# Kernel optimization log

Hardware: AMD Instinct MI355X
Metric: run time of the kernel (lower is better)

The kernel has to match this reference:

```python
import jax, jax.numpy as jnp
import numpy as np

N = 100000          # num nodes
E_C = 6_400_000     # connection edges
E_D = 400_000       # destination edges
F_IN = 5
H = 8
BN_EPS = 1e-5
L2_EPS = 1e-12


def setup_inputs() -> dict:
    key = jax.random.key(0)
    ks = jax.random.split(key, 16)
    d = {}
    d["x"] = jax.random.normal(ks[0], (N, F_IN), dtype=jnp.float32)
    d["edge_index_connections"] = jax.random.randint(ks[1], (2, E_C), 0, N, dtype=jnp.int64)
    d["edge_index_destinations"] = jax.random.randint(ks[2], (2, E_D), 0, N, dtype=jnp.int64)
    # SAGEConv weights: lin_l (neighbor aggregate), lin_r (root), no bias
    d["W1l"] = jax.random.normal(ks[3], (H, F_IN), jnp.float32) * 0.3
    d["W1r"] = jax.random.normal(ks[4], (H, F_IN), jnp.float32) * 0.3
    d["W2l"] = jax.random.normal(ks[5], (H, H), jnp.float32) * 0.3
    d["W2r"] = jax.random.normal(ks[6], (H, H), jnp.float32) * 0.3
    d["W3l"] = jax.random.normal(ks[7], (H, H), jnp.float32) * 0.3
    d["W3r"] = jax.random.normal(ks[8], (H, H), jnp.float32) * 0.3
    d["W4l"] = jax.random.normal(ks[9], (H, H), jnp.float32) * 0.3
    d["W4r"] = jax.random.normal(ks[10], (H, H), jnp.float32) * 0.3
    # LazyBatchNorm1d affine params (init gamma=1, beta=0)
    for i in range(1, 5):
        d[f"g{i}"] = jnp.ones((H,), jnp.float32)
        d[f"b{i}"] = jnp.zeros((H,), jnp.float32)
    return d


def _sage(x, ei, Wl, Wr):
    # PyG SAGEConv(mean aggr, normalize=True, bias=False):
    # out = lin_l(mean_{j in N(i)} x_j) + lin_r(x_i); then L2 normalize rows.
    src, dst = ei[0], ei[1]
    msgs = x[src]                                            # [E, F] gather
    s = jax.ops.segment_sum(msgs, dst, num_segments=N)       # [N, F]
    cnt = jax.ops.segment_sum(jnp.ones((ei.shape[1],), x.dtype), dst, num_segments=N)
    mean = s / jnp.maximum(cnt, 1.0)[:, None]                # zero for isolated nodes
    out = mean @ Wl.T + x @ Wr.T                             # [N, H]
    nrm = jnp.linalg.norm(out, axis=-1, keepdims=True)
    return out / jnp.maximum(nrm, L2_EPS)


def _bn(x, g, b):
    # BatchNorm1d in training mode: per-feature batch stats (biased variance)
    m = x.mean(axis=0)
    v = x.var(axis=0)
    return (x - m) * jax.lax.rsqrt(v + BN_EPS) * g + b


def reference(x, edge_index_connections, edge_index_destinations,
              W1l, W1r, W2l, W2r, W3l, W3r, W4l, W4r,
              g1, b1, g2, b2, g3, b3, g4, b4):
    eic = edge_index_connections
    eid = edge_index_destinations
    h = _bn(jax.nn.relu(_sage(x, eic, W1l, W1r)), g1, b1)
    # ITERATIONS_BEFORE_DESTINATION = 1 (conv4 + bn2)
    h = _bn(jax.nn.relu(_sage(h, eic, W4l, W4r)), g2, b2)
    # destination pass (conv2 + bn3)
    h = _bn(jax.nn.relu(_sage(h, eid, W2l, W2r)), g3, b3)
    # ITERATIONS_AFTER_DESTINATION = 2 (conv3 + bn4)
    for _ in range(2):
        h = _bn(jax.nn.relu(_sage(h, eic, W3l, W3r)), g4, b4)
    return h
```

## Files before the change

### kernel.cpp

```cpp
#include <hip/hip_runtime.h>
#include <hip/hip_fp16.h>

#define NN 100000
#define EC 6400000
#define ED 400000
#define BN_EPS 1e-5f
#define NSB ((NN + 255) >> 8)
#define NCH 256
#define CSR_CAP 19200
#define CHUNK_OF(E) (((((E) + NCH - 1) / NCH) + 3) & ~3)


__global__ __launch_bounds__(1024)
void pre_hist_prep(const int* __restrict__ eic, const int* __restrict__ eid,
                   int* __restrict__ bhist_c, int* __restrict__ bhist_d,
                   const float* __restrict__ x, const float* __restrict__ W1l,
                   const float* __restrict__ W1r, float* __restrict__ xp,
                   __half* __restrict__ xp16,
                   float* __restrict__ W1lp, float* __restrict__ W1rp) {
    int blk = blockIdx.x;
    if (blk < 2 * NCH) {
        const int* ei = (blk < NCH) ? eic : eid;
        int E = (blk < NCH) ? EC : ED;
        int* bhist = (blk < NCH) ? bhist_c : bhist_d;
        int k = (blk < NCH) ? blk : blk - NCH;
        __shared__ int h[NSB];
        for (int i = threadIdx.x; i < NSB; i += 1024) h[i] = 0;
        __syncthreads();
        int chunk = CHUNK_OF(E);
        int beg = k * chunk, end = min(E, beg + chunk);
        for (int e = beg + threadIdx.x * 4; e < end; e += 1024 * 4) {
            int4 d4 = *(const int4*)&ei[E + e];
            atomicAdd(&h[d4.x >> 8], 1);
            atomicAdd(&h[d4.y >> 8], 1);
            atomicAdd(&h[d4.z >> 8], 1);
            atomicAdd(&h[d4.w >> 8], 1);
        }
        __syncthreads();
        for (int i = threadIdx.x; i < NSB; i += 1024) bhist[i * NCH + k] = h[i];
    } else {
        int pb = blk - 2 * NCH;
        int t = pb * 1024 + threadIdx.x;
        if (t < 64) {
            int f = t >> 3, k = t & 7;
            W1lp[t] = (k < 5) ? W1l[f * 5 + k] : 0.f;
            W1rp[t] = (k < 5) ? W1r[f * 5 + k] : 0.f;
        }
        for (int idx = t; idx < NN * 8; idx += 32 * 1024) {
            int f = idx & 7, i = idx >> 3;
            float v = (f < 5) ? x[i * 5 + f] : 0.f;
            xp[idx] = v;
            xp16[idx] = __float2half(v);
        }
    }
}

__global__ __launch_bounds__(256)
void row_scan2(int* __restrict__ bhist_c, int* __restrict__ total_c,
               int* __restrict__ bhist_d, int* __restrict__ total_d) {
    int blk = blockIdx.x;
    int* row = (blk < NSB) ? (bhist_c + blk * NCH)
                           : (bhist_d + (blk - NSB) * NCH);
    int* total = (blk < NSB) ? total_c : total_d;
    int bb = (blk < NSB) ? blk : blk - NSB;
    __shared__ int wsum[4];
    int lane = threadIdx.x & 63, w = threadIdx.x >> 6;
    int v = row[threadIdx.x];
    int x = v;
    #pragma unroll
    for (int sh = 1; sh < 64; sh <<= 1) { int y = __shfl_up(x, sh); if (lane >= sh) x += y; }
    if (lane == 63) wsum[w] = x;
    __syncthreads();
    int wb = 0;
    #pragma unroll
    for (int j = 0; j < 4; ++j) if (j < w) wb += wsum[j];
    row[threadIdx.x] = wb + x - v;
    if (threadIdx.x == 255) total[bb] = wb + x;
}

__global__ void base2(const int* __restrict__ total_c, int* __restrict__ bbase_c,
                      const int* __restrict__ total_d, int* __restrict__ bbase_d,
                      float* __restrict__ stats) {
    for (int i = threadIdx.x; i < 5 * 256; i += 256) stats[i] = 0.f;
    __shared__ int wsum[4];
    __shared__ int carry;
    int lane = threadIdx.x & 63, w = threadIdx.x >> 6;
    for (int which = 0; which < 2; ++which) {
        const int* gt = which ? total_d : total_c;
        int* bb = which ? bbase_d : bbase_c;
        if (threadIdx.x == 0) carry = 0;
        __syncthreads();
        for (int s = 0; s < NSB; s += 256) {
            int idx = s + threadIdx.x;
            int v = (idx < NSB) ? gt[idx] : 0;
            int x = v;
            #pragma unroll
            for (int sh = 1; sh < 64; sh <<= 1) { int y = __shfl_up(x, sh); if (lane >= sh) x += y; }
            if (lane == 63) wsum[w] = x;
            __syncthreads();
            int wb = 0;
            #pragma unroll
            for (int j = 0; j < 4; ++j) if (j < w) wb += wsum[j];
            int all = wsum[0] + wsum[1] + wsum[2] + wsum[3];
            if (idx < NSB) bb[idx] = carry + wb + x - v;
            __syncthreads();
            if (threadIdx.x == 0) carry += all;
            __syncthreads();
        }
    }
}

__global__ __launch_bounds__(1024)
void scatter2(const int* __restrict__ eic, const int* __restrict__ eid,
              const int* __restrict__ bhist_c, const int* __restrict__ bbase_c,
              unsigned* __restrict__ packed_c,
              const int* __restrict__ bhist_d, const int* __restrict__ bbase_d,
              unsigned* __restrict__ packed_d) {
    int blk = blockIdx.x;
    const int* ei = (blk < NCH) ? eic : eid;
    int E = (blk < NCH) ? EC : ED;
    const int* bhist = (blk < NCH) ? bhist_c : bhist_d;
    const int* bbase = (blk < NCH) ? bbase_c : bbase_d;
    unsigned* packed = (blk < NCH) ? packed_c : packed_d;
    int k = (blk < NCH) ? blk : blk - NCH;
    __shared__ int cur[NSB];
    for (int b = threadIdx.x; b < NSB; b += 1024)
        cur[b] = bbase[b] + bhist[b * NCH + k];
    __syncthreads();
    int chunk = CHUNK_OF(E);
    int beg = k * chunk, end = min(E, beg + chunk);
    for (int e = beg + threadIdx.x * 4; e < end; e += 1024 * 4) {
        int4 s4 = *(const int4*)&ei[e];
        int4 d4 = *(const int4*)&ei[E + e];
        { int p = atomicAdd(&cur[d4.x >> 8], 1); packed[p] = (unsigned)s4.x | ((unsigned)(d4.x & 255) << 17); }
        { int p = atomicAdd(&cur[d4.y >> 8], 1); packed[p] = (unsigned)s4.y | ((unsigned)(d4.y & 255) << 17); }
        { int p = atomicAdd(&cur[d4.z >> 8], 1); packed[p] = (unsigned)s4.z | ((unsigned)(d4.z & 255) << 17); }
        { int p = atomicAdd(&cur[d4.w >> 8], 1); packed[p] = (unsigned)s4.w | ((unsigned)(d4.w & 255) << 17); }
    }
}

__global__ __launch_bounds__(256)
void csr2(const unsigned* __restrict__ packed_c, const int* __restrict__ bbase_c,
          const int* __restrict__ total_c, int* __restrict__ csr_c,
          int* __restrict__ offs_c, int* __restrict__ deg_c, float* __restrict__ inv_c,
          const unsigned* __restrict__ packed_d, const int* __restrict__ bbase_d,
          const int* __restrict__ total_d, int* __restrict__ csr_d,
          int* __restrict__ offs_d, int* __restrict__ deg_d, float* __restrict__ inv_d) {
    int blk = blockIdx.x;
    const unsigned* packed = (blk < NSB) ? packed_c : packed_d;
    const int* bbase = (blk < NSB) ? bbase_c : bbase_d;
    const int* total = (blk < NSB) ? total_c : total_d;
    int* csr  = (blk < NSB) ? csr_c : csr_d;
    int* offs = (blk < NSB) ? offs_c : offs_d;
    int* deg  = (blk < NSB) ? deg_c : deg_d;
    float* inv = (blk < NSB) ? inv_c : inv_d;
    int b = (blk < NSB) ? blk : blk - NSB;

    __shared__ int h[256];
    __shared__ int loff[256];
    __shared__ int ws2[4];
    __shared__ int ebuf[CSR_CAP];
    int ebeg = bbase[b], ecnt = total[b];
    int node0 = b << 8;
    int nn = min(256, NN - node0);
    h[threadIdx.x] = 0;
    __syncthreads();
    for (int e = threadIdx.x; e < ecnt; e += 256)
        atomicAdd(&h[packed[ebeg + e] >> 17], 1);
    __syncthreads();
    {
        int lane = threadIdx.x & 63, w = threadIdx.x >> 6;
        int v = h[threadIdx.x], x = v;
        #pragma unroll
        for (int sh = 1; sh < 64; sh <<= 1) { int y = __shfl_up(x, sh); if (lane >= sh) x += y; }
        if (lane == 63) ws2[w] = x;
        __syncthreads();
        int wb = 0;
        #pragma unroll
        for (int j = 0; j < 4; ++j) if (j < w) wb += ws2[j];
        int excl = wb + x - v;
        loff[threadIdx.x] = excl;
        if (threadIdx.x < nn) {
            int node = node0 + threadIdx.x;
            offs[node] = ebeg + excl;
            deg[node]  = v;
            inv[node]  = 1.0f / (float)(v > 1 ? v : 1);
        }
    }
    __syncthreads();
    if (ecnt <= CSR_CAP) {
        for (int e = threadIdx.x; e < ecnt; e += 256) {
            unsigned u = packed[ebeg + e];
            int p = atomicAdd(&loff[u >> 17], 1);
            ebuf[p] = (int)(u & 0x1FFFF);
        }
        __syncthreads();
        for (int e = threadIdx.x; e < ecnt; e += 256) csr[ebeg + e] = ebuf[e];
    } else {
        for (int e = threadIdx.x; e < ecnt; e += 256) {
            unsigned u = packed[ebeg + e];
            int p = atomicAdd(&loff[u >> 17], 1);
            csr[ebeg + p] = (int)(u & 0x1FFFF);
        }
    }
}

#define ACC8(RV, M) do { \
    float2 q0 = __half22float2(*(const __half2*)&RV.x); \
    float2 q1 = __half22float2(*(const __half2*)&RV.y); \
    float2 q2 = __half22float2(*(const __half2*)&RV.z); \
    float2 q3 = __half22float2(*(const __half2*)&RV.w); \
    a0 = fmaf(q0.x, M, a0); a1 = fmaf(q0.y, M, a1); \
    a2 = fmaf(q1.x, M, a2); a3 = fmaf(q1.y, M, a3); \
    a4 = fmaf(q2.x, M, a4); a5 = fmaf(q2.y, M, a5); \
    a6 = fmaf(q3.x, M, a6); a7 = fmaf(q3.y, M, a7); \
} while (0)

template<bool APPLY_BN>
__global__ __launch_bounds__(256)
void sage_layer8(const float* __restrict__ hin,
                 const __half* __restrict__ hin16,
                 const float* __restrict__ stats_in,
                 const float* __restrict__ gin, const float* __restrict__ bin,
                 const int* __restrict__ offs, const int* __restrict__ deg,
                 const int* __restrict__ csr, const float* __restrict__ inv,
                 const float* __restrict__ Wl, const float* __restrict__ Wr,
                 float* __restrict__ hout, __half* __restrict__ hout16,
                 float* __restrict__ stats_out) {
    __shared__ float bl[16];
    int tid = threadIdx.x;
    if (tid < 16) bl[tid] = 0.f;
    __syncthreads();
    int wave = tid >> 6, lane = tid & 63, g = lane >> 3, f = lane & 7;

    float wls[8], wrs[8];
    float Bl = 0.f, Br = 0.f;
    #pragma unroll
    for (int k = 0; k < 8; ++k) {
        float w_l = Wl[f * 8 + k], w_r = Wr[f * 8 + k];
        float sck = 1.f, shk = 0.f;
        if constexpr (APPLY_BN) {
            float m = stats_in[k * 16] * (1.f / NN);
            float v = stats_in[(8 + k) * 16] * (1.f / NN) - m * m;
            float is = rsqrtf(v + BN_EPS);
            sck = gin[k] * is;
            shk = bin[k] - m * sck;
        }
        wls[k] = sck * w_l;
        wrs[k] = sck * w_r;
        Bl = fmaf(shk, w_l, Bl);
        Br = fmaf(shk, w_r, Br);
    }

    float acc_r = 0.f, acc_r2 = 0.f;
    const int stride = gridDim.x * 32;
    for (int i0 = (blockIdx.x * 4 + wave) * 8; i0 < NN; i0 += stride) {
        int i = i0 + g;
        int ic = min(i, NN - 1);
        bool ok = (i < NN);
        int d = ok ? deg[ic] : 0;
        int o = offs[ic];
        float im = inv[ic];
        const float4* hp = (const float4*)(hin + (size_t)ic * 8);
        float4 h0 = hp[0];
        float4 h1 = hp[1];
        float a0 = 0, a1 = 0, a2 = 0, a3 = 0, a4 = 0, a5 = 0, a6 = 0, a7 = 0;
        for (int b = 0; b < d; b += 32) {
            int e = b + f * 4;
            const int* cp = csr + o + e;
            int c0 = cp[0], c1 = cp[1], c2 = cp[2], c3 = cp[3];
            bool k0 = (e < d), k1 = (e + 1 < d), k2 = (e + 2 < d), k3 = (e + 3 < d);
            unsigned s0 = k0 ? ((unsigned)c0 & 0x1FFFFu) : 0u;
            unsigned s1 = k1 ? ((unsigned)c1 & 0x1FFFFu) : 0u;
            unsigned s2 = k2 ? ((unsigned)c2 & 0x1FFFFu) : 0u;
            unsigned s3 = k3 ? ((unsigned)c3 & 0x1FFFFu) : 0u;
            uint4 r0 = *(const uint4*)(hin16 + (size_t)s0 * 8);
            uint4 r1 = *(const uint4*)(hin16 + (size_t)s1 * 8);
            uint4 r2 = *(const uint4*)(hin16 + (size_t)s2 * 8);
            uint4 r3 = *(const uint4*)(hin16 + (size_t)s3 * 8);
            float m0 = k0 ? 1.f : 0.f;
            float m1 = k1 ? 1.f : 0.f;
            float m2 = k2 ? 1.f : 0.f;
            float m3 = k3 ? 1.f : 0.f;
            ACC8(r0, m0);
            ACC8(r1, m1);
            ACC8(r2, m2);
            ACC8(r3, m3);
        }
        #pragma unroll
        for (int msk = 1; msk < 8; msk <<= 1) {
            a0 += __shfl_xor(a0, msk); a1 += __shfl_xor(a1, msk);
            a2 += __shfl_xor(a2, msk); a3 += __shfl_xor(a3, msk);
            a4 += __shfl_xor(a4, msk); a5 += __shfl_xor(a5, msk);
            a6 += __shfl_xor(a6, msk); a7 += __shfl_xor(a7, msk);
        }
        float dnz = (d > 0) ? 1.f : 0.f;
        float hk[8] = { h0.x, h0.y, h0.z, h0.w, h1.x, h1.y, h1.z, h1.w };
        float ac[8] = { a0, a1, a2, a3, a4, a5, a6, a7 };
        float y = fmaf(dnz, Bl, Br);
        #pragma unroll
        for (int k = 0; k < 8; ++k) {
            y = fmaf(ac[k] * im, wls[k], y);
            y = fmaf(hk[k], wrs[k], y);
        }
        float n2 = y * y;
        n2 += __shfl_xor(n2, 1);
        n2 += __shfl_xor(n2, 2);
        n2 += __shfl_xor(n2, 4);
        float z = y / fmaxf(sqrtf(n2), 1e-12f);
        float r = fmaxf(z, 0.f);
        r = ok ? r : 0.f;
        if (ok) {
            hout[(size_t)i * 8 + f] = r;
            hout16[(size_t)i * 8 + f] = __float2half(r);
        }
        acc_r += r;
        acc_r2 += r * r;
    }
    atomicAdd(&bl[f], acc_r);
    atomicAdd(&bl[8 + f], acc_r2);
    __syncthreads();
    if (tid < 16) atomicAdd(&stats_out[tid * 16], bl[tid]);
}

__global__ void apply_bn_out(const float* __restrict__ hin,
                             const float* __restrict__ stats,
                             const float* __restrict__ g, const float* __restrict__ b,
                             float* __restrict__ out) {
    int t = blockIdx.x * blockDim.x + threadIdx.x;
    if (t >= NN * 8) return;
    int f = t & 7;
    float m = stats[f * 16] * (1.0f / NN);
    float v = stats[(8 + f) * 16] * (1.0f / NN) - m * m;
    float sc = g[f] * rsqrtf(v + BN_EPS);
    float sh = b[f] - m * sc;
    out[t] = fmaf(hin[t], sc, sh);
}


static inline char* bump(char*& p, size_t bytes) {
    char* r = p;
    p += (bytes + 255) & ~(size_t)255;
    return r;
}

extern "C" void kernel_launch(void* const* d_in, const int* in_sizes, int n_in,
                              void* d_out, int out_size, void* d_ws, size_t ws_size,
                              hipStream_t stream) {
    const float* x   = (const float*)d_in[0];
    const int* eic   = (const int*)d_in[1];
    const int* eid   = (const int*)d_in[2];
    const float* W1l = (const float*)d_in[3];
    const float* W1r = (const float*)d_in[4];
    const float* W2l = (const float*)d_in[5];
    const float* W2r = (const float*)d_in[6];
    const float* W3l = (const float*)d_in[7];
    const float* W3r = (const float*)d_in[8];
    const float* W4l = (const float*)d_in[9];
    const float* W4r = (const float*)d_in[10];
    const float* g1 = (const float*)d_in[11];
    const float* b1 = (const float*)d_in[12];
    const float* g2 = (const float*)d_in[13];
    const float* b2 = (const float*)d_in[14];
    const float* g3 = (const float*)d_in[15];
    const float* b3 = (const float*)d_in[16];
    const float* g4 = (const float*)d_in[17];
    const float* b4 = (const float*)d_in[18];
    float* out = (float*)d_out;

    char* p = (char*)d_ws;
    float* stats   = (float*)bump(p, 5 * 256 * 4);
    int*   bhist_c = (int*)  bump(p, (size_t)NSB * NCH * 4);
    int*   bhist_d = (int*)  bump(p, (size_t)NSB * NCH * 4);
    int*   total_c = (int*)  bump(p, NSB * 4);
    int*   bbase_c = (int*)  bump(p, NSB * 4);
    int*   total_d = (int*)  bump(p, NSB * 4);
    int*   bbase_d = (int*)  bump(p, NSB * 4);
    int*   offs_c  = (int*)  bump(p, NN * 4);
    int*   deg_c   = (int*)  bump(p, NN * 4);
    float* inv_c   = (float*)bump(p, NN * 4);
    int*   offs_d  = (int*)  bump(p, NN * 4);
    int*   deg_d   = (int*)  bump(p, NN * 4);
    float* inv_d   = (float*)bump(p, NN * 4);
    int*   csr_c   = (int*)  bump(p, ((size_t)EC + 64) * 4);
    int*   csr_d   = (int*)  bump(p, ((size_t)ED + 64) * 4);
    float* xp32    = (float*)bump(p, (size_t)NN * 8 * 4);
    __half* xp16   = (__half*)bump(p, (size_t)NN * 8 * 2);
    float* W1lp    = (float*)bump(p, 64 * 4);
    float* W1rp    = (float*)bump(p, 64 * 4);
    unsigned* packed_d = (unsigned*)bump(p, (size_t)ED * 4);
    char* pc = p;
    unsigned* packed_c = (unsigned*)bump(p, (size_t)EC * 4);
    char* pr = pc;
    float*  r_a   = (float*) bump(pr, (size_t)NN * 8 * 4);
    float*  r_b   = (float*) bump(pr, (size_t)NN * 8 * 4);
    __half* h16_a = (__half*)bump(pr, (size_t)NN * 8 * 2);
    __half* h16_b = (__half*)bump(pr, (size_t)NN * 8 * 2);
    (void)ws_size; (void)in_sizes; (void)n_in; (void)out_size;

    pre_hist_prep<<<2 * NCH + 32, 1024, 0, stream>>>(
        eic, eid, bhist_c, bhist_d, x, W1l, W1r, xp32, xp16, W1lp, W1rp);
    row_scan2<<<2 * NSB, 256, 0, stream>>>(bhist_c, total_c, bhist_d, total_d);
    base2<<<1, 256, 0, stream>>>(total_c, bbase_c, total_d, bbase_d, stats);
    scatter2<<<2 * NCH, 1024, 0, stream>>>(
        eic, eid, bhist_c, bbase_c, packed_c, bhist_d, bbase_d, packed_d);
    csr2<<<2 * NSB, 256, 0, stream>>>(
        packed_c, bbase_c, total_c, csr_c, offs_c, deg_c, inv_c,
        packed_d, bbase_d, total_d, csr_d, offs_d, deg_d, inv_d);

    const int LB = 2048;
    sage_layer8<false><<<LB, 256, 0, stream>>>(
        xp32, xp16, nullptr, nullptr, nullptr,
        offs_c, deg_c, csr_c, inv_c, W1lp, W1rp, r_a, h16_a, stats + 0);
    sage_layer8<true><<<LB, 256, 0, stream>>>(
        r_a, h16_a, stats + 0, g1, b1,
        offs_c, deg_c, csr_c, inv_c, W4l, W4r, r_b, h16_b, stats + 256);
    sage_layer8<true><<<LB, 256, 0, stream>>>(
        r_b, h16_b, stats + 256, g2, b2,
        offs_d, deg_d, csr_d, inv_d, W2l, W2r, r_a, h16_a, stats + 512);
    sage_layer8<true><<<LB, 256, 0, stream>>>(
        r_a, h16_a, stats + 512, g3, b3,
        offs_c, deg_c, csr_c, inv_c, W3l, W3r, r_b, h16_b, stats + 768);
    sage_layer8<true><<<LB, 256, 0, stream>>>(
        r_b, h16_b, stats + 768, g4, b4,
        offs_c, deg_c, csr_c, inv_c, W3l, W3r, r_a, h16_a, stats + 1024);
    apply_bn_out<<<(NN * 8 + 255) / 256, 256, 0, stream>>>(r_a, stats + 1024, g4, b4, out);
}
```

Baseline: 580.6 us.

## Launch one node-group per wave, widen gather to 8 edges per lane with CSR prefetch

Swaps the grid-stride loop over nodes in the SAGE layer for a grid of exactly NN/32 blocks, so each wave handles one group of 8 nodes with no bounds checks. Each lane now gathers 8 neighbour rows per iteration (64 edges per node-group step) and prefetches the next CSR indices in a software-pipelined way, giving more memory-level parallelism. Per-thread BN-stat accumulation becomes direct shared atomics per node. The CSR buffers gain extra padding for the wider over-read. The change relies on NN being divisible by 32 and adds register pressure plus more blocks and LDS atomics.

```diff
diff --git a/kernel.cpp b/kernel.cpp
--- a/kernel.cpp
+++ b/kernel.cpp
@@ -252,73 +252,82 @@
         Br = fmaf(shk, w_r, Br);
     }
 
-    float acc_r = 0.f, acc_r2 = 0.f;
-    const int stride = gridDim.x * 32;
-    for (int i0 = (blockIdx.x * 4 + wave) * 8; i0 < NN; i0 += stride) {
-        int i = i0 + g;
-        int ic = min(i, NN - 1);
-        bool ok = (i < NN);
-        int d = ok ? deg[ic] : 0;
-        int o = offs[ic];
-        float im = inv[ic];
-        const float4* hp = (const float4*)(hin + (size_t)ic * 8);
-        float4 h0 = hp[0];
-        float4 h1 = hp[1];
-        float a0 = 0, a1 = 0, a2 = 0, a3 = 0, a4 = 0, a5 = 0, a6 = 0, a7 = 0;
-        for (int b = 0; b < d; b += 32) {
-            int e = b + f * 4;
-            const int* cp = csr + o + e;
-            int c0 = cp[0], c1 = cp[1], c2 = cp[2], c3 = cp[3];
-            bool k0 = (e < d), k1 = (e + 1 < d), k2 = (e + 2 < d), k3 = (e + 3 < d);
-            unsigned s0 = k0 ? ((unsigned)c0 & 0x1FFFFu) : 0u;
-            unsigned s1 = k1 ? ((unsigned)c1 & 0x1FFFFu) : 0u;
-            unsigned s2 = k2 ? ((unsigned)c2 & 0x1FFFFu) : 0u;
-            unsigned s3 = k3 ? ((unsigned)c3 & 0x1FFFFu) : 0u;
-            uint4 r0 = *(const uint4*)(hin16 + (size_t)s0 * 8);
-            uint4 r1 = *(const uint4*)(hin16 + (size_t)s1 * 8);
-            uint4 r2 = *(const uint4*)(hin16 + (size_t)s2 * 8);
-            uint4 r3 = *(const uint4*)(hin16 + (size_t)s3 * 8);
-            float m0 = k0 ? 1.f : 0.f;
-            float m1 = k1 ? 1.f : 0.f;
-            float m2 = k2 ? 1.f : 0.f;
-            float m3 = k3 ? 1.f : 0.f;
-            ACC8(r0, m0);
-            ACC8(r1, m1);
-            ACC8(r2, m2);
-            ACC8(r3, m3);
-        }
-        #pragma unroll
-        for (int msk = 1; msk < 8; msk <<= 1) {
-            a0 += __shfl_xor(a0, msk); a1 += __shfl_xor(a1, msk);
-            a2 += __shfl_xor(a2, msk); a3 += __shfl_xor(a3, msk);
-            a4 += __shfl_xor(a4, msk); a5 += __shfl_xor(a5, msk);
-            a6 += __shfl_xor(a6, msk); a7 += __shfl_xor(a7, msk);
-        }
-        float dnz = (d > 0) ? 1.f : 0.f;
-        float hk[8] = { h0.x, h0.y, h0.z, h0.w, h1.x, h1.y, h1.z, h1.w };
-        float ac[8] = { a0, a1, a2, a3, a4, a5, a6, a7 };
-        float y = fmaf(dnz, Bl, Br);
-        #pragma unroll
-        for (int k = 0; k < 8; ++k) {
-            y = fmaf(ac[k] * im, wls[k], y);
-            y = fmaf(hk[k], wrs[k], y);
-        }
-        float n2 = y * y;
-        n2 += __shfl_xor(n2, 1);
-        n2 += __shfl_xor(n2, 2);
-        n2 += __shfl_xor(n2, 4);
-        float z = y / fmaxf(sqrtf(n2), 1e-12f);
-        float r = fmaxf(z, 0.f);
-        r = ok ? r : 0.f;
-        if (ok) {
-            hout[(size_t)i * 8 + f] = r;
-            hout16[(size_t)i * 8 + f] = __float2half(r);
-        }
-        acc_r += r;
-        acc_r2 += r * r;
-    }
-    atomicAdd(&bl[f], acc_r);
-    atomicAdd(&bl[8 + f], acc_r2);
+    int i = (blockIdx.x * 4 + wave) * 8 + g;
+    int d = deg[i];
+    int o = offs[i];
+    float im = inv[i];
+    const float4* hp = (const float4*)(hin + (size_t)i * 8);
+    float4 h0 = hp[0];
+    float4 h1 = hp[1];
+
+    float a0 = 0, a1 = 0, a2 = 0, a3 = 0, a4 = 0, a5 = 0, a6 = 0, a7 = 0;
+    const int* cp = csr + o + f * 8;
+    int c0 = cp[0], c1 = cp[1], c2 = cp[2], c3 = cp[3];
+    int c4 = cp[4], c5 = cp[5], c6 = cp[6], c7 = cp[7];
+    for (int b = 0; b < d; b += 64) {
+        int bp = (b + 64 < d) ? (b + 64) : 0;
+        int n0 = cp[bp],     n1 = cp[bp + 1], n2 = cp[bp + 2], n3 = cp[bp + 3];
+        int n4 = cp[bp + 4], n5 = cp[bp + 5], n6 = cp[bp + 6], n7 = cp[bp + 7];
+        int e = b + f * 8;
+        bool k0 = (e < d),     k1 = (e + 1 < d), k2 = (e + 2 < d), k3 = (e + 3 < d);
+        bool k4 = (e + 4 < d), k5 = (e + 5 < d), k6 = (e + 6 < d), k7 = (e + 7 < d);
+        unsigned s0 = k0 ? ((unsigned)c0 & 0x1FFFFu) : 0u;
+        unsigned s1 = k1 ? ((unsigned)c1 & 0x1FFFFu) : 0u;
+        unsigned s2 = k2 ? ((unsigned)c2 & 0x1FFFFu) : 0u;
+        unsigned s3 = k3 ? ((unsigned)c3 & 0x1FFFFu) : 0u;
+        unsigned s4 = k4 ? ((unsigned)c4 & 0x1FFFFu) : 0u;
+        unsigned s5 = k5 ? ((unsigned)c5 & 0x1FFFFu) : 0u;
+        unsigned s6 = k6 ? ((unsigned)c6 & 0x1FFFFu) : 0u;
+        unsigned s7 = k7 ? ((unsigned)c7 & 0x1FFFFu) : 0u;
+        uint4 r0 = *(const uint4*)(hin16 + (size_t)s0 * 8);
+        uint4 r1 = *(const uint4*)(hin16 + (size_t)s1 * 8);
+        uint4 r2 = *(const uint4*)(hin16 + (size_t)s2 * 8);
+        uint4 r3 = *(const uint4*)(hin16 + (size_t)s3 * 8);
+        uint4 r4 = *(const uint4*)(hin16 + (size_t)s4 * 8);
+        uint4 r5 = *(const uint4*)(hin16 + (size_t)s5 * 8);
+        uint4 r6 = *(const uint4*)(hin16 + (size_t)s6 * 8);
+        uint4 r7 = *(const uint4*)(hin16 + (size_t)s7 * 8);
+        float m0 = k0 ? 1.f : 0.f, m1 = k1 ? 1.f : 0.f;
+        float m2 = k2 ? 1.f : 0.f, m3 = k3 ? 1.f : 0.f;
+        float m4 = k4 ? 1.f : 0.f, m5 = k5 ? 1.f : 0.f;
+        float m6 = k6 ? 1.f : 0.f, m7 = k7 ? 1.f : 0.f;
+        ACC8(r0, m0);
+        ACC8(r1, m1);
+        ACC8(r2, m2);
+        ACC8(r3, m3);
+        ACC8(r4, m4);
+        ACC8(r5, m5);
+        ACC8(r6, m6);
+        ACC8(r7, m7);
+        c0 = n0; c1 = n1; c2 = n2; c3 = n3;
+        c4 = n4; c5 = n5; c6 = n6; c7 = n7;
+    }
+    #pragma unroll
+    for (int msk = 1; msk < 8; msk <<= 1) {
+        a0 += __shfl_xor(a0, msk); a1 += __shfl_xor(a1, msk);
+        a2 += __shfl_xor(a2, msk); a3 += __shfl_xor(a3, msk);
+        a4 += __shfl_xor(a4, msk); a5 += __shfl_xor(a5, msk);
+        a6 += __shfl_xor(a6, msk); a7 += __shfl_xor(a7, msk);
+    }
+    float dnz = (d > 0) ? 1.f : 0.f;
+    float hk[8] = { h0.x, h0.y, h0.z, h0.w, h1.x, h1.y, h1.z, h1.w };
+    float ac[8] = { a0, a1, a2, a3, a4, a5, a6, a7 };
+    float y = fmaf(dnz, Bl, Br);
+    #pragma unroll
+    for (int k = 0; k < 8; ++k) {
+        y = fmaf(ac[k] * im, wls[k], y);
+        y = fmaf(hk[k], wrs[k], y);
+    }
+    float n2 = y * y;
+    n2 += __shfl_xor(n2, 1);
+    n2 += __shfl_xor(n2, 2);
+    n2 += __shfl_xor(n2, 4);
+    float z = y / fmaxf(sqrtf(n2), 1e-12f);
+    float r = fmaxf(z, 0.f);
+    hout[(size_t)i * 8 + f] = r;
+    hout16[(size_t)i * 8 + f] = __float2half(r);
+    atomicAdd(&bl[f], r);
+    atomicAdd(&bl[8 + f], r * r);
     __syncthreads();
     if (tid < 16) atomicAdd(&stats_out[tid * 16], bl[tid]);
 }
@@ -382,8 +391,8 @@
     int*   offs_d  = (int*)  bump(p, NN * 4);
     int*   deg_d   = (int*)  bump(p, NN * 4);
     float* inv_d   = (float*)bump(p, NN * 4);
-    int*   csr_c   = (int*)  bump(p, ((size_t)EC + 64) * 4);
-    int*   csr_d   = (int*)  bump(p, ((size_t)ED + 64) * 4);
+    int*   csr_c   = (int*)  bump(p, ((size_t)EC + 256) * 4);
+    int*   csr_d   = (int*)  bump(p, ((size_t)ED + 256) * 4);
     float* xp32    = (float*)bump(p, (size_t)NN * 8 * 4);
     __half* xp16   = (__half*)bump(p, (size_t)NN * 8 * 2);
     float* W1lp    = (float*)bump(p, 64 * 4);
@@ -408,7 +417,7 @@
         packed_c, bbase_c, total_c, csr_c, offs_c, deg_c, inv_c,
         packed_d, bbase_d, total_d, csr_d, offs_d, deg_d, inv_d);
 
-    const int LB = 2048;
+    const int LB = NN / 32;
     sage_layer8<false><<<LB, 256, 0, stream>>>(
         xp32, xp16, nullptr, nullptr, nullptr,
         offs_c, deg_c, csr_c, inv_c, W1lp, W1rp, r_a, h16_a, stats + 0);
```

Result: slower. 675.2 us (+16.3%).

## Build CSR via global per-node degree atomics instead of bucketed two-pass sort

Applied to the files above, without the earlier changes.

Replaces the two-level bucket sort (per-chunk LDS histograms, scatter into packed buckets, then a per-bucket local CSR build) with direct global atomics: per-node degree counting, a two-level prefix scan over nodes, and a scatter that writes each source index straight into its CSR slot. This removes the packed intermediate array and the shared-memory CSR pass. In exchange it relies on millions of global atomics to random addresses, which may contend or run slower than LDS atomics. It also writes CSR entries in random order, so neighbour order within a row is no longer deterministic.

```diff
diff --git a/kernel.cpp b/kernel.cpp
--- a/kernel.cpp
+++ b/kernel.cpp
@@ -5,48 +5,50 @@
 #define EC 6400000
 #define ED 400000
 #define BN_EPS 1e-5f
-#define NSB ((NN + 255) >> 8)
-#define NCH 256
-#define CSR_CAP 19200
-#define CHUNK_OF(E) (((((E) + NCH - 1) / NCH) + 3) & ~3)
-
-
-__global__ __launch_bounds__(1024)
-void pre_hist_prep(const int* __restrict__ eic, const int* __restrict__ eid,
-                   int* __restrict__ bhist_c, int* __restrict__ bhist_d,
-                   const float* __restrict__ x, const float* __restrict__ W1l,
-                   const float* __restrict__ W1r, float* __restrict__ xp,
-                   __half* __restrict__ xp16,
-                   float* __restrict__ W1lp, float* __restrict__ W1rp) {
+#define HB_C 1563
+#define HB_D 98
+#define SC 98
+#define PREP_B 32
+
+
+__global__ __launch_bounds__(1024)
+void zero_init(int* __restrict__ deg_c, int* __restrict__ deg_d,
+               float* __restrict__ stats) {
+    int t = blockIdx.x * 1024 + threadIdx.x;
+    for (int i = t; i < NN; i += 64 * 1024) { deg_c[i] = 0; deg_d[i] = 0; }
+    if (t < 5 * 256) stats[t] = 0.f;
+}
+
+__global__ __launch_bounds__(1024)
+void hist_prep(const int* __restrict__ eic, const int* __restrict__ eid,
+               int* __restrict__ deg_c, int* __restrict__ deg_d,
+               const float* __restrict__ x, const float* __restrict__ W1l,
+               const float* __restrict__ W1r, float* __restrict__ xp,
+               __half* __restrict__ xp16,
+               float* __restrict__ W1lp, float* __restrict__ W1rp) {
     int blk = blockIdx.x;
-    if (blk < 2 * NCH) {
-        const int* ei = (blk < NCH) ? eic : eid;
-        int E = (blk < NCH) ? EC : ED;
-        int* bhist = (blk < NCH) ? bhist_c : bhist_d;
-        int k = (blk < NCH) ? blk : blk - NCH;
-        __shared__ int h[NSB];
-        for (int i = threadIdx.x; i < NSB; i += 1024) h[i] = 0;
-        __syncthreads();
-        int chunk = CHUNK_OF(E);
-        int beg = k * chunk, end = min(E, beg + chunk);
-        for (int e = beg + threadIdx.x * 4; e < end; e += 1024 * 4) {
+    if (blk < HB_C + HB_D) {
+        const int* ei = (blk < HB_C) ? eic : eid;
+        int E = (blk < HB_C) ? EC : ED;
+        int* deg = (blk < HB_C) ? deg_c : deg_d;
+        int base = (blk < HB_C) ? blk : blk - HB_C;
+        int e = (base * 1024 + threadIdx.x) * 4;
+        if (e < E) {
             int4 d4 = *(const int4*)&ei[E + e];
-            atomicAdd(&h[d4.x >> 8], 1);
-            atomicAdd(&h[d4.y >> 8], 1);
-            atomicAdd(&h[d4.z >> 8], 1);
-            atomicAdd(&h[d4.w >> 8], 1);
-        }
-        __syncthreads();
-        for (int i = threadIdx.x; i < NSB; i += 1024) bhist[i * NCH + k] = h[i];
+            atomicAdd(&deg[d4.x], 1);
+            atomicAdd(&deg[d4.y], 1);
+            atomicAdd(&deg[d4.z], 1);
+            atomicAdd(&deg[d4.w], 1);
+        }
     } else {
-        int pb = blk - 2 * NCH;
+        int pb = blk - (HB_C + HB_D);
         int t = pb * 1024 + threadIdx.x;
         if (t < 64) {
             int f = t >> 3, k = t & 7;
             W1lp[t] = (k < 5) ? W1l[f * 5 + k] : 0.f;
             W1rp[t] = (k < 5) ? W1r[f * 5 + k] : 0.f;
         }
-        for (int idx = t; idx < NN * 8; idx += 32 * 1024) {
+        for (int idx = t; idx < NN * 8; idx += PREP_B * 1024) {
             int f = idx & 7, i = idx >> 3;
             float v = (f < 5) ? x[i * 5 + f] : 0.f;
             xp[idx] = v;
@@ -55,17 +57,20 @@
     }
 }
 
-__global__ __launch_bounds__(256)
-void row_scan2(int* __restrict__ bhist_c, int* __restrict__ total_c,
-               int* __restrict__ bhist_d, int* __restrict__ total_d) {
+__global__ __launch_bounds__(1024)
+void scan_deg(const int* __restrict__ deg_c, int* __restrict__ offs_c,
+              int* __restrict__ btot_c,
+              const int* __restrict__ deg_d, int* __restrict__ offs_d,
+              int* __restrict__ btot_d) {
     int blk = blockIdx.x;
-    int* row = (blk < NSB) ? (bhist_c + blk * NCH)
-                           : (bhist_d + (blk - NSB) * NCH);
-    int* total = (blk < NSB) ? total_c : total_d;
-    int bb = (blk < NSB) ? blk : blk - NSB;
-    __shared__ int wsum[4];
+    const int* deg = (blk < SC) ? deg_c : deg_d;
+    int* offs = (blk < SC) ? offs_c : offs_d;
+    int* btot = (blk < SC) ? btot_c : btot_d;
+    int b = (blk < SC) ? blk : blk - SC;
+    int n = b * 1024 + threadIdx.x;
+    int v = (n < NN) ? deg[n] : 0;
+    __shared__ int wsum[16];
     int lane = threadIdx.x & 63, w = threadIdx.x >> 6;
-    int v = row[threadIdx.x];
     int x = v;
     #pragma unroll
     for (int sh = 1; sh < 64; sh <<= 1) { int y = __shfl_up(x, sh); if (lane >= sh) x += y; }
@@ -73,135 +78,76 @@
     __syncthreads();
     int wb = 0;
     #pragma unroll
-    for (int j = 0; j < 4; ++j) if (j < w) wb += wsum[j];
-    row[threadIdx.x] = wb + x - v;
-    if (threadIdx.x == 255) total[bb] = wb + x;
-}
-
-__global__ void base2(const int* __restrict__ total_c, int* __restrict__ bbase_c,
-                      const int* __restrict__ total_d, int* __restrict__ bbase_d,
-                      float* __restrict__ stats) {
-    for (int i = threadIdx.x; i < 5 * 256; i += 256) stats[i] = 0.f;
-    __shared__ int wsum[4];
-    __shared__ int carry;
+    for (int j = 0; j < 16; ++j) if (j < w) wb += wsum[j];
+    if (n < NN) offs[n] = wb + x - v;
+    if (threadIdx.x == 1023) btot[b] = wb + x;
+}
+
+__global__ void scan_base(const int* __restrict__ btot_c, int* __restrict__ bbase_c,
+                          const int* __restrict__ btot_d, int* __restrict__ bbase_d) {
+    __shared__ int wsum[2];
     int lane = threadIdx.x & 63, w = threadIdx.x >> 6;
     for (int which = 0; which < 2; ++which) {
-        const int* gt = which ? total_d : total_c;
+        const int* bt = which ? btot_d : btot_c;
         int* bb = which ? bbase_d : bbase_c;
-        if (threadIdx.x == 0) carry = 0;
+        int v = (threadIdx.x < SC) ? bt[threadIdx.x] : 0;
+        int x = v;
+        #pragma unroll
+        for (int sh = 1; sh < 64; sh <<= 1) { int y = __shfl_up(x, sh); if (lane >= sh) x += y; }
+        if (lane == 63) wsum[w] = x;
         __syncthreads();
-        for (int s = 0; s < NSB; s += 256) {
-            int idx = s + threadIdx.x;
-            int v = (idx < NSB) ? gt[idx] : 0;
-            int x = v;
-            #pragma unroll
-            for (int sh = 1; sh < 64; sh <<= 1) { int y = __shfl_up(x, sh); if (lane >= sh) x += y; }
-            if (lane == 63) wsum[w] = x;
-            __syncthreads();
-            int wb = 0;
-            #pragma unroll
-            for (int j = 0; j < 4; ++j) if (j < w) wb += wsum[j];
-            int all = wsum[0] + wsum[1] + wsum[2] + wsum[3];
-            if (idx < NSB) bb[idx] = carry + wb + x - v;
-            __syncthreads();
-            if (threadIdx.x == 0) carry += all;
-            __syncthreads();
-        }
-    }
-}
-
-__global__ __launch_bounds__(1024)
-void scatter2(const int* __restrict__ eic, const int* __restrict__ eid,
-              const int* __restrict__ bhist_c, const int* __restrict__ bbase_c,
-              unsigned* __restrict__ packed_c,
-              const int* __restrict__ bhist_d, const int* __restrict__ bbase_d,
-              unsigned* __restrict__ packed_d) {
+        int wb = (w == 1) ? wsum[0] : 0;
+        if (threadIdx.x < SC) bb[threadIdx.x] = wb + x - v;
+        __syncthreads();
+    }
+}
+
+__global__ __launch_bounds__(1024)
+void finalize_offs(int* __restrict__ offs_c, const int* __restrict__ bbase_c,
+                   const int* __restrict__ deg_c, int* __restrict__ cur_c,
+                   float* __restrict__ inv_c,
+                   int* __restrict__ offs_d, const int* __restrict__ bbase_d,
+                   const int* __restrict__ deg_d, int* __restrict__ cur_d,
+                   float* __restrict__ inv_d) {
     int blk = blockIdx.x;
-    const int* ei = (blk < NCH) ? eic : eid;
-    int E = (blk < NCH) ? EC : ED;
-    const int* bhist = (blk < NCH) ? bhist_c : bhist_d;
-    const int* bbase = (blk < NCH) ? bbase_c : bbase_d;
-    unsigned* packed = (blk < NCH) ? packed_c : packed_d;
-    int k = (blk < NCH) ? blk : blk - NCH;
-    __shared__ int cur[NSB];
-    for (int b = threadIdx.x; b < NSB; b += 1024)
-        cur[b] = bbase[b] + bhist[b * NCH + k];
-    __syncthreads();
-    int chunk = CHUNK_OF(E);
-    int beg = k * chunk, end = min(E, beg + chunk);
-    for (int e = beg + threadIdx.x * 4; e < end; e += 1024 * 4) {
+    int* offs = (blk < SC) ? offs_c : offs_d;
+    const int* bbase = (blk < SC) ? bbase_c : bbase_d;
+    const int* deg = (blk < SC) ? deg_c : deg_d;
+    int* cur = (blk < SC) ? cur_c : cur_d;
+    float* inv = (blk < SC) ? inv_c : inv_d;
+    int b = (blk < SC) ? blk : blk - SC;
+    int n = b * 1024 + threadIdx.x;
+    if (n < NN) {
+        int o = offs[n] + bbase[b];
+        offs[n] = o;
+        cur[n] = o;
+        int d = deg[n];
+        inv[n] = 1.0f / (float)(d > 1 ? d : 1);
+    }
+}
+
+__global__ __launch_bounds__(1024)
+void scatter_csr(const int* __restrict__ eic, const int* __restrict__ eid,
+                 int* __restrict__ cur_c, int* __restrict__ cur_d,
+                 int* __restrict__ csr_c, int* __restrict__ csr_d) {
+    int blk = blockIdx.x;
+    const int* ei = (blk < HB_C) ? eic : eid;
+    int E = (blk < HB_C) ? EC : ED;
+    int* cur = (blk < HB_C) ? cur_c : cur_d;
+    int* csr = (blk < HB_C) ? csr_c : csr_d;
+    int base = (blk < HB_C) ? blk : blk - HB_C;
+    int e = (base * 1024 + threadIdx.x) * 4;
+    if (e < E) {
         int4 s4 = *(const int4*)&ei[e];
         int4 d4 = *(const int4*)&ei[E + e];
-        { int p = atomicAdd(&cur[d4.x >> 8], 1); packed[p] = (unsigned)s4.x | ((unsigned)(d4.x & 255) << 17); }
-        { int p = atomicAdd(&cur[d4.y >> 8], 1); packed[p] = (unsigned)s4.y | ((unsigned)(d4.y & 255) << 17); }
-        { int p = atomicAdd(&cur[d4.z >> 8], 1); packed[p] = (unsigned)s4.z | ((unsigned)(d4.z & 255) << 17); }
-        { int p = atomicAdd(&cur[d4.w >> 8], 1); packed[p] = (unsigned)s4.w | ((unsigned)(d4.w & 255) << 17); }
-    }
-}
-
-__global__ __launch_bounds__(256)
-void csr2(const unsigned* __restrict__ packed_c, const int* __restrict__ bbase_c,
-          const int* __restrict__ total_c, int* __restrict__ csr_c,
-          int* __restrict__ offs_c, int* __restrict__ deg_c, float* __restrict__ inv_c,
-          const unsigned* __restrict__ packed_d, const int* __restrict__ bbase_d,
-          const int* __restrict__ total_d, int* __restrict__ csr_d,
-          int* __restrict__ offs_d, int* __restrict__ deg_d, float* __restrict__ inv_d) {
-    int blk = blockIdx.x;
-    const unsigned* packed = (blk < NSB) ? packed_c : packed_d;
-    const int* bbase = (blk < NSB) ? bbase_c : bbase_d;
-    const int* total = (blk < NSB) ? total_c : total_d;
-    int* csr  = (blk < NSB) ? csr_c : csr_d;
-    int* offs = (blk < NSB) ? offs_c : offs_d;
-    int* deg  = (blk < NSB) ? deg_c : deg_d;
-    float* inv = (blk < NSB) ? inv_c : inv_d;
-    int b = (blk < NSB) ? blk : blk - NSB;
-
-    __shared__ int h[256];
-    __shared__ int loff[256];
-    __shared__ int ws2[4];
-    __shared__ int ebuf[CSR_CAP];
-    int ebeg = bbase[b], ecnt = total[b];
-    int node0 = b << 8;
-    int nn = min(256, NN - node0);
-    h[threadIdx.x] = 0;
-    __syncthreads();
-    for (int e = threadIdx.x; e < ecnt; e += 256)
-        atomicAdd(&h[packed[ebeg + e] >> 17], 1);
-    __syncthreads();
-    {
-        int lane = threadIdx.x & 63, w = threadIdx.x >> 6;
-        int v = h[threadIdx.x], x = v;
-        #pragma unroll
-        for (int sh = 1; sh < 64; sh <<= 1) { int y = __shfl_up(x, sh); if (lane >= sh) x += y; }
-        if (lane == 63) ws2[w] = x;
-        __syncthreads();
-        int wb = 0;
-        #pragma unroll
-        for (int j = 0; j < 4; ++j) if (j < w) wb += ws2[j];
-        int excl = wb + x - v;
-        loff[threadIdx.x] = excl;
-        if (threadIdx.x < nn) {
-            int node = node0 + threadIdx.x;
-            offs[node] = ebeg + excl;
-            deg[node]  = v;
-            inv[node]  = 1.0f / (float)(v > 1 ? v : 1);
-        }
-    }
-    __syncthreads();
-    if (ecnt <= CSR_CAP) {
-        for (int e = threadIdx.x; e < ecnt; e += 256) {
-            unsigned u = packed[ebeg + e];
-            int p = atomicAdd(&loff[u >> 17], 1);
-            ebuf[p] = (int)(u & 0x1FFFF);
-        }
-        __syncthreads();
-        for (int e = threadIdx.x; e < ecnt; e += 256) csr[ebeg + e] = ebuf[e];
-    } else {
-        for (int e = threadIdx.x; e < ecnt; e += 256) {
-            unsigned u = packed[ebeg + e];
-            int p = atomicAdd(&loff[u >> 17], 1);
-            csr[ebeg + p] = (int)(u & 0x1FFFF);
-        }
+        int p0 = atomicAdd(&cur[d4.x], 1);
+        int p1 = atomicAdd(&cur[d4.y], 1);
+        int p2 = atomicAdd(&cur[d4.z], 1);
+        int p3 = atomicAdd(&cur[d4.w], 1);
+        csr[p0] = s4.x;
+        csr[p1] = s4.y;
+        csr[p2] = s4.z;
+        csr[p3] = s4.w;
     }
 }
 
@@ -370,43 +316,39 @@
 
     char* p = (char*)d_ws;
     float* stats   = (float*)bump(p, 5 * 256 * 4);
-    int*   bhist_c = (int*)  bump(p, (size_t)NSB * NCH * 4);
-    int*   bhist_d = (int*)  bump(p, (size_t)NSB * NCH * 4);
-    int*   total_c = (int*)  bump(p, NSB * 4);
-    int*   bbase_c = (int*)  bump(p, NSB * 4);
-    int*   total_d = (int*)  bump(p, NSB * 4);
-    int*   bbase_d = (int*)  bump(p, NSB * 4);
+    int*   deg_c   = (int*)  bump(p, NN * 4);
     int*   offs_c  = (int*)  bump(p, NN * 4);
-    int*   deg_c   = (int*)  bump(p, NN * 4);
     float* inv_c   = (float*)bump(p, NN * 4);
+    int*   cur_c   = (int*)  bump(p, NN * 4);
+    int*   deg_d   = (int*)  bump(p, NN * 4);
     int*   offs_d  = (int*)  bump(p, NN * 4);
-    int*   deg_d   = (int*)  bump(p, NN * 4);
     float* inv_d   = (float*)bump(p, NN * 4);
-    int*   csr_c   = (int*)  bump(p, ((size_t)EC + 64) * 4);
-    int*   csr_d   = (int*)  bump(p, ((size_t)ED + 64) * 4);
+    int*   cur_d   = (int*)  bump(p, NN * 4);
+    int*   btot_c  = (int*)  bump(p, 128 * 4);
+    int*   bbase_c = (int*)  bump(p, 128 * 4);
+    int*   btot_d  = (int*)  bump(p, 128 * 4);
+    int*   bbase_d = (int*)  bump(p, 128 * 4);
+    int*   csr_c   = (int*)  bump(p, ((size_t)EC + 256) * 4);
+    int*   csr_d   = (int*)  bump(p, ((size_t)ED + 256) * 4);
     float* xp32    = (float*)bump(p, (size_t)NN * 8 * 4);
     __half* xp16   = (__half*)bump(p, (size_t)NN * 8 * 2);
     float* W1lp    = (float*)bump(p, 64 * 4);
     float* W1rp    = (float*)bump(p, 64 * 4);
-    unsigned* packed_d = (unsigned*)bump(p, (size_t)ED * 4);
-    char* pc = p;
-    unsigned* packed_c = (unsigned*)bump(p, (size_t)EC * 4);
-    char* pr = pc;
-    float*  r_a   = (float*) bump(pr, (size_t)NN * 8 * 4);
-    float*  r_b   = (float*) bump(pr, (size_t)NN * 8 * 4);
-    __half* h16_a = (__half*)bump(pr, (size_t)NN * 8 * 2);
-    __half* h16_b = (__half*)bump(pr, (size_t)NN * 8 * 2);
+    float*  r_a   = (float*) bump(p, (size_t)NN * 8 * 4);
+    float*  r_b   = (float*) bump(p, (size_t)NN * 8 * 4);
+    __half* h16_a = (__half*)bump(p, (size_t)NN * 8 * 2);
+    __half* h16_b = (__half*)bump(p, (size_t)NN * 8 * 2);
     (void)ws_size; (void)in_sizes; (void)n_in; (void)out_size;
 
-    pre_hist_prep<<<2 * NCH + 32, 1024, 0, stream>>>(
-        eic, eid, bhist_c, bhist_d, x, W1l, W1r, xp32, xp16, W1lp, W1rp);
-    row_scan2<<<2 * NSB, 256, 0, stream>>>(bhist_c, total_c, bhist_d, total_d);
-    base2<<<1, 256, 0, stream>>>(total_c, bbase_c, total_d, bbase_d, stats);
-    scatter2<<<2 * NCH, 1024, 0, stream>>>(
-        eic, eid, bhist_c, bbase_c, packed_c, bhist_d, bbase_d, packed_d);
-    csr2<<<2 * NSB, 256, 0, stream>>>(
-        packed_c, bbase_c, total_c, csr_c, offs_c, deg_c, inv_c,
-        packed_d, bbase_d, total_d, csr_d, offs_d, deg_d, inv_d);
+    zero_init<<<64, 1024, 0, stream>>>(deg_c, deg_d, stats);
+    hist_prep<<<HB_C + HB_D + PREP_B, 1024, 0, stream>>>(
+        eic, eid, deg_c, deg_d, x, W1l, W1r, xp32, xp16, W1lp, W1rp);
+    scan_deg<<<2 * SC, 1024, 0, stream>>>(deg_c, offs_c, btot_c, deg_d, offs_d, btot_d);
+    scan_base<<<1, 128, 0, stream>>>(btot_c, bbase_c, btot_d, bbase_d);
+    finalize_offs<<<2 * SC, 1024, 0, stream>>>(
+        offs_c, bbase_c, deg_c, cur_c, inv_c,
+        offs_d, bbase_d, deg_d, cur_d, inv_d);
+    scatter_csr<<<HB_C + HB_D, 1024, 0, stream>>>(eic, eid, cur_c, cur_d, csr_c, csr_d);
 
     const int LB = 2048;
     sage_layer8<false><<<LB, 256, 0, stream>>>(
```

Measured after the change: 1.339 ms. +130.6%, slower.
